# Optimization experiments

Hardware: AMD Instinct MI355X
Metric: run time of the kernel (lower is better)

## Reference

```python
import jax, jax.numpy as jnp
import numpy as np

INPUT_DIM = 512
HIDDEN_DIM = 1024
OUTPUT_DIM = 128
BATCH = 128
SEQ_LEN = 512


def setup_inputs() -> dict:
    key = jax.random.key(0)
    ks = jax.random.split(key, 8)
    s_ih = 1.0 / np.sqrt(HIDDEN_DIM)
    x = jax.random.normal(ks[0], (BATCH, SEQ_LEN, INPUT_DIM), dtype=jnp.float32)
    # LSTMCell params (PyTorch layout: [4*H, in], gate order i,f,g,o)
    W_ih = jax.random.uniform(ks[1], (4 * HIDDEN_DIM, INPUT_DIM), jnp.float32, -s_ih, s_ih)
    W_hh = jax.random.uniform(ks[2], (4 * HIDDEN_DIM, HIDDEN_DIM), jnp.float32, -s_ih, s_ih)
    b_ih = jax.random.uniform(ks[3], (4 * HIDDEN_DIM,), jnp.float32, -s_ih, s_ih)
    b_hh = jax.random.uniform(ks[4], (4 * HIDDEN_DIM,), jnp.float32, -s_ih, s_ih)
    # fc: Linear(hidden_dim, output_dim)
    s_fc = 1.0 / np.sqrt(HIDDEN_DIM)
    W_fc = jax.random.uniform(ks[5], (OUTPUT_DIM, HIDDEN_DIM), jnp.float32, -s_fc, s_fc)
    b_fc = jax.random.uniform(ks[6], (OUTPUT_DIM,), jnp.float32, -s_fc, s_fc)
    return {"x": x, "W_ih": W_ih, "W_hh": W_hh, "b_ih": b_ih, "b_hh": b_hh,
            "W_fc": W_fc, "b_fc": b_fc}


def _lstm_forward(x, W_ih, W_hh, b_ih, b_hh):
    B = x.shape[0]
    H = W_hh.shape[1]
    # Precompute input projections for all timesteps: [S, B, 4H]
    x_proj = jnp.einsum('bsi,gi->sbg', x, W_ih) + b_ih + b_hh

    def step(carry, xp_t):
        h, c = carry
        gates = xp_t + h @ W_hh.T  # [B, 4H]
        i, f, g, o = jnp.split(gates, 4, axis=-1)
        i = jax.nn.sigmoid(i)
        f = jax.nn.sigmoid(f)
        g = jnp.tanh(g)
        o = jax.nn.sigmoid(o)
        c = f * c + i * g
        h = o * jnp.tanh(c)
        return (h, c), None

    h0 = jnp.zeros((B, H), x.dtype)
    c0 = jnp.zeros((B, H), x.dtype)
    (hn, cn), _ = jax.lax.scan(step, (h0, c0), x_proj)
    return hn


def reference(x, W_ih, W_hh, b_ih, b_hh, W_fc, b_fc):
    hn = _lstm_forward(x, W_ih, W_hh, b_ih, b_hh)
    return hn @ W_fc.T + b_fc
```

## Files before the change

### kernel.cpp

```cpp
#include <hip/hip_runtime.h>
#include <hip/hip_bf16.h>

#define B_   128
#define S_   512
#define I_   512
#define H_   1024
#define G_   4096
#define O_   128
#define NWG  256
#define HU   8

typedef short bf16x8 __attribute__((ext_vector_type(8)));
typedef float f32x4  __attribute__((ext_vector_type(4)));
typedef unsigned short u16;
typedef unsigned long long u64;

__device__ __forceinline__ u16 f2bf(float f){
  union { float f; unsigned u; } v; v.f = f;
  unsigned r = v.u + 0x7fffu + ((v.u >> 16) & 1u);
  return (u16)(r >> 16);
}
__device__ __forceinline__ float sigm(float x){ return 1.0f/(1.0f + __expf(-x)); }
__device__ __forceinline__ float tanhfast(float x){ return 1.0f - 2.0f/(1.0f + __expf(2.0f*x)); }

__device__ __forceinline__ void coh_store64(u16* p, u64 v){
  __hip_atomic_store((u64*)p, v, __ATOMIC_RELAXED, __HIP_MEMORY_SCOPE_AGENT);
}
__device__ __forceinline__ u64 coh_load64(const void* p){
  return __hip_atomic_load((const u64*)p, __ATOMIC_RELAXED, __HIP_MEMORY_SCOPE_AGENT);
}

#define HL(dst, boff) \
  asm volatile("global_load_dwordx4 %0, %1, off offset:" boff " sc0 sc1" \
               : "=v"(dst) : "v"(haddr) : "memory");

#define MF(a,b,c) __builtin_amdgcn_mfma_f32_16x16x32_bf16((a),(b),(c),0,0,0)

__global__ void cast_f32_bf16(const float* __restrict__ src, u16* __restrict__ dst, int n4){
  int i = blockIdx.x*blockDim.x + threadIdx.x;
  const int st = gridDim.x*blockDim.x;
  for (; i < n4; i += st){
    float4 v = ((const float4*)src)[i];
    ushort4 o = make_ushort4(f2bf(v.x), f2bf(v.y), f2bf(v.z), f2bf(v.w));
    ((ushort4*)dst)[i] = o;
  }
}

__global__ void prep_bias(const float* __restrict__ bih, const float* __restrict__ bhh,
                          float* __restrict__ bc){
  int i = blockIdx.x*blockDim.x + threadIdx.x;
  if (i < G_) bc[i] = bih[i] + bhh[i];
}

__shared__ u16 wih_s[32*520];
__shared__ u16 whh_s[32*1032];

__global__ __launch_bounds__(256) void lstm_persist(
    const u16*   __restrict__ xbf,
    const float* __restrict__ xf,
    const int use_xbf,
    const u16*   __restrict__ Wih,
    const u16*   __restrict__ Whh,
    const float* __restrict__ bias,
    u16*         __restrict__ hbuf,
    float*       __restrict__ hfin,
    const float* __restrict__ Wfc,
    const float* __restrict__ bfc,
    float*       __restrict__ out,
    unsigned*    __restrict__ bar)
{
  const int wg = blockIdx.x, tid = threadIdx.x;
  const int bh = wg >> 7;
  const int cg = wg & 127;
  const int wv = tid >> 6, lane = tid & 63;
  const int n = lane & 15, g4 = lane >> 4;
  const int u0 = cg * HU;
  const int rb = bh*64 + wv*16;

  auto colmap = [&](int lc){ return (((lc>>4)<<1) + ((lc&15)>>3))*H_ + u0 + (lc&7); };

  for (int idx = tid; idx < 32*64; idx += 256){
    int lc = idx >> 6, c8 = (idx & 63) * 8;
    *(bf16x8*)(&wih_s[lc*520 + c8]) = *(const bf16x8*)(Wih + (size_t)colmap(lc)*I_ + c8);
  }
  for (int idx = tid; idx < 32*128; idx += 256){
    int lc = idx >> 7, c8 = (idx & 127) * 8;
    *(bf16x8*)(&whh_s[lc*1032 + c8]) = *(const bf16x8*)(Whh + (size_t)colmap(lc)*H_ + c8);
  }
  if (tid < 64){
    u16* p = hbuf + (size_t)(bh*64 + tid)*H_ + u0;
    coh_store64(p, 0ull); coh_store64(p + 4, 0ull);
  }
  asm volatile("s_waitcnt vmcnt(0)" ::: "memory");
  __syncthreads();
  if (tid == 0) __hip_atomic_fetch_add(bar, 1u, __ATOMIC_RELAXED, __HIP_MEMORY_SCOPE_AGENT);

  const float bias0 = bias[(0*2 + (n>>3))*H_ + u0 + (n&7)];
  const float bias1 = bias[(1*2 + (n>>3))*H_ + u0 + (n&7)];
  float cst[4] = {0.f, 0.f, 0.f, 0.f};
  const int hi = (n >> 3);
  const f32x4 z = {0.f,0.f,0.f,0.f};
  f32x4 ax0, ax1;

  auto xpart = [&](int t){
    ax0 = z; ax1 = z;
    if (use_xbf){
      const u16* xr = xbf + (size_t)(rb + n)*(S_*I_) + (size_t)t*I_;
      #pragma unroll 4
      for (int ks = 0; ks < 16; ++ks){
        const int kk = ks*32 + g4*8;
        bf16x8 a  = *(const bf16x8*)(xr + kk);
        bf16x8 b0 = *(const bf16x8*)(&wih_s[n*520 + kk]);
        bf16x8 b1 = *(const bf16x8*)(&wih_s[(16+n)*520 + kk]);
        ax0 = MF(a, b0, ax0); ax1 = MF(a, b1, ax1);
      }
    } else {
      const float* xr = xf + (size_t)(rb + n)*(S_*I_) + (size_t)t*I_;
      #pragma unroll 2
      for (int ks = 0; ks < 16; ++ks){
        const int kk = ks*32 + g4*8;
        float4 va = *(const float4*)(xr + kk), vb = *(const float4*)(xr + kk + 4);
        bf16x8 a;
        a[0]=(short)f2bf(va.x); a[1]=(short)f2bf(va.y); a[2]=(short)f2bf(va.z); a[3]=(short)f2bf(va.w);
        a[4]=(short)f2bf(vb.x); a[5]=(short)f2bf(vb.y); a[6]=(short)f2bf(vb.z); a[7]=(short)f2bf(vb.w);
        bf16x8 b0 = *(const bf16x8*)(&wih_s[n*520 + kk]);
        bf16x8 b1 = *(const bf16x8*)(&wih_s[(16+n)*520 + kk]);
        ax0 = MF(a, b0, ax0); ax1 = MF(a, b1, ax1);
      }
    }
  };

  xpart(0);
  unsigned tgt = NWG;

  for (int t = 0; t < S_; ++t){
    const u16* __restrict__ hc = hbuf + (size_t)(t & 1)*(B_*H_);
    u16*       __restrict__ hn = hbuf + (size_t)((t+1) & 1)*(B_*H_);

    if (tid == 0){
      while (__hip_atomic_load(bar, __ATOMIC_RELAXED, __HIP_MEMORY_SCOPE_AGENT) < tgt)
        __builtin_amdgcn_s_sleep(1);
    }
    __syncthreads();

    const u16* haddr = hc + (size_t)(rb + n)*H_ + g4*8;
    f32x4 acc0a = ax0, acc1a = ax1, acc0b = z, acc1b = z;
    bf16x8 hA0,hA1,hA2,hA3,hA4,hA5,hA6,hA7;
    bf16x8 hB0,hB1,hB2,hB3,hB4,hB5,hB6,hB7;

    #define CONS(hreg, ks) { \
      const int kk = (ks)*32 + g4*8; \
      bf16x8 bf0 = *(const bf16x8*)(&whh_s[n*1032 + kk]); \
      bf16x8 bf1 = *(const bf16x8*)(&whh_s[(16+n)*1032 + kk]); \
      if ((ks) & 1){ acc0b = MF(hreg, bf0, acc0b); acc1b = MF(hreg, bf1, acc1b); } \
      else         { acc0a = MF(hreg, bf0, acc0a); acc1a = MF(hreg, bf1, acc1a); } }
    #define CONS8(P, base) \
      CONS(P##0, (base)+0) CONS(P##1, (base)+1) CONS(P##2, (base)+2) CONS(P##3, (base)+3) \
      CONS(P##4, (base)+4) CONS(P##5, (base)+5) CONS(P##6, (base)+6) CONS(P##7, (base)+7)

    HL(hA0,"0")    HL(hA1,"64")   HL(hA2,"128")  HL(hA3,"192")
    HL(hA4,"256")  HL(hA5,"320")  HL(hA6,"384")  HL(hA7,"448")
    HL(hB0,"512")  HL(hB1,"576")  HL(hB2,"640")  HL(hB3,"704")
    HL(hB4,"768")  HL(hB5,"832")  HL(hB6,"896")  HL(hB7,"960")

    asm volatile("s_waitcnt vmcnt(8)" ::: "memory");
    __builtin_amdgcn_sched_barrier(0);
    CONS8(hA, 0)
    HL(hA0,"1024") HL(hA1,"1088") HL(hA2,"1152") HL(hA3,"1216")
    HL(hA4,"1280") HL(hA5,"1344") HL(hA6,"1408") HL(hA7,"1472")

    asm volatile("s_waitcnt vmcnt(8)" ::: "memory");
    __builtin_amdgcn_sched_barrier(0);
    CONS8(hB, 8)
    HL(hB0,"1536") HL(hB1,"1600") HL(hB2,"1664") HL(hB3,"1728")
    HL(hB4,"1792") HL(hB5,"1856") HL(hB6,"1920") HL(hB7,"1984")

    asm volatile("s_waitcnt vmcnt(8)" ::: "memory");
    __builtin_amdgcn_sched_barrier(0);
    CONS8(hA, 16)

    asm volatile("s_waitcnt vmcnt(0)" ::: "memory");
    __builtin_amdgcn_sched_barrier(0);
    CONS8(hB, 24)

    #undef CONS8
    #undef CONS

    f32x4 acc0 = acc0a + acc0b;
    f32x4 acc1 = acc1a + acc1b;

    #pragma unroll
    for (int reg = 0; reg < 4; ++reg){
      float p0 = acc0[reg] + bias0;
      float p1 = acc1[reg] + bias1;
      float q0 = __shfl_xor(p0, 8);
      float q1 = __shfl_xor(p1, 8);
      float ip = hi ? q0 : p0;
      float fp = hi ? p0 : q0;
      float gp = hi ? q1 : p1;
      float op = hi ? p1 : q1;
      float iv = sigm(ip), fv = sigm(fp), gv = tanhfast(gp), ov = sigm(op);
      float c = fv*cst[reg] + iv*gv;
      cst[reg] = c;
      float h = ov * tanhfast(c);
      const int r = rb + g4*4 + reg;

      unsigned v16 = f2bf(h);
      unsigned pr  = v16 | (__shfl_xor(v16, 1) << 16);
      unsigned pr2 = __shfl_xor(pr, 2);
      if (hi == 0 && (n & 3) == 0){
        u64 q = (u64)pr | ((u64)pr2 << 32);
        coh_store64(hn + (size_t)r*H_ + u0 + n, q);
      }
      if (t == S_-1){
        unsigned fb = __float_as_uint(h);
        unsigned fo = __shfl_xor(fb, 1);
        if (hi == 0 && (n & 1) == 0){
          u64 q = (u64)fb | ((u64)fo << 32);
          __hip_atomic_store((u64*)(hfin + (size_t)r*H_ + u0 + n), q,
                             __ATOMIC_RELAXED, __HIP_MEMORY_SCOPE_AGENT);
        }
      }
    }

    asm volatile("s_waitcnt vmcnt(0)" ::: "memory");
    __syncthreads();
    if (tid == 0) __hip_atomic_fetch_add(bar, 1u, __ATOMIC_RELAXED, __HIP_MEMORY_SCOPE_AGENT);
    tgt += NWG;

    if (t < S_-1) xpart(t+1);
  }

  if (tid == 0){
    while (__hip_atomic_load(bar, __ATOMIC_RELAXED, __HIP_MEMORY_SCOPE_AGENT) < tgt)
      __builtin_amdgcn_s_sleep(1);
  }
  __syncthreads();

  {
    const int b = wg & 127;
    const int o = (wg >> 7)*64 + (tid >> 2);
    const int qtr = tid & 3;
    const float* hb = hfin + (size_t)b*H_ + qtr*256;
    const float* wb = Wfc + (size_t)o*H_ + qtr*256;
    float s = 0.f;
    #pragma unroll 8
    for (int j = 0; j < 128; ++j){
      u64 q = coh_load64(hb + j*2);
      float a0 = __uint_as_float((unsigned)q);
      float a1 = __uint_as_float((unsigned)(q >> 32));
      float2 w = *(const float2*)(wb + j*2);
      s += a0*w.x + a1*w.y;
    }
    s += __shfl_xor(s, 1);
    s += __shfl_xor(s, 2);
    if (qtr == 0) out[(size_t)b*O_ + o] = s + bfc[o];
  }
}

extern "C" void kernel_launch(void* const* d_in, const int* in_sizes, int n_in,
                              void* d_out, int out_size, void* d_ws, size_t ws_size,
                              hipStream_t stream) {
  const float* x   = (const float*)d_in[0];
  const float* Wih = (const float*)d_in[1];
  const float* Whh = (const float*)d_in[2];
  const float* bih = (const float*)d_in[3];
  const float* bhh = (const float*)d_in[4];
  const float* Wfc = (const float*)d_in[5];
  const float* bfc = (const float*)d_in[6];
  float* out = (float*)d_out;

  char* ws = (char*)d_ws;
  u16*      wih_bf = (u16*)     (ws + 0);
  u16*      whh_bf = (u16*)     (ws + 4194304);
  float*    biasc  = (float*)   (ws + 12582912);
  u16*      hbuf   = (u16*)     (ws + 12599296);
  float*    hfin   = (float*)   (ws + 13123584);
  unsigned* bar    = (unsigned*)(ws + 13647872);
  u16*      xbf    = (u16*)     (ws + 13648128);
  const int use_xbf = (ws_size >= (size_t)13648128 + 67108864) ? 1 : 0;

  hipMemsetAsync(bar, 0, 256, stream);
  cast_f32_bf16<<<1024, 256, 0, stream>>>(Wih, wih_bf, (G_*I_)/4);
  cast_f32_bf16<<<2048, 256, 0, stream>>>(Whh, whh_bf, (G_*H_)/4);
  prep_bias<<<16, 256, 0, stream>>>(bih, bhh, biasc);
  if (use_xbf)
    cast_f32_bf16<<<2048, 256, 0, stream>>>(x, xbf, (B_*S_*I_)/4);

  lstm_persist<<<NWG, 256, 0, stream>>>(xbf, x, use_xbf, wih_bf, whh_bf, biasc,
                                        hbuf, hfin, Wfc, bfc, out, bar);
}
```

Measured before the change: 4.748 ms.

## Replace atomic-counter grid barrier with per-workgroup flags and issue all h loads upfront

The single global counter that all 256 workgroups atomically incremented each timestep is replaced by one flag per workgroup. Each workgroup stores its step number into its own flag, and all 256 threads poll one flag each, combining the results with a wave-wide __all. This removes contention on a single atomic address in the per-step grid barrier. Separately, all 32 hidden-state loads are now issued before any MFMA, using staged vmcnt waits, which deepens memory-level parallelism at the cost of more VGPRs.

```diff
diff --git a/kernel.cpp b/kernel.cpp
--- a/kernel.cpp
+++ b/kernel.cpp
@@ -67,7 +67,7 @@
     const float* __restrict__ Wfc,
     const float* __restrict__ bfc,
     float*       __restrict__ out,
-    unsigned*    __restrict__ bar)
+    unsigned*    __restrict__ flags)
 {
   const int wg = blockIdx.x, tid = threadIdx.x;
   const int bh = wg >> 7;
@@ -79,6 +79,16 @@
 
   auto colmap = [&](int lc){ return (((lc>>4)<<1) + ((lc&15)>>3))*H_ + u0 + (lc&7); };
 
+  const unsigned* myflag = flags + (wv<<6) + lane;
+  auto waitbar = [&](unsigned tgt){
+    unsigned f = __hip_atomic_load(myflag, __ATOMIC_RELAXED, __HIP_MEMORY_SCOPE_AGENT);
+    while (!__all((int)(f >= tgt))){
+      __builtin_amdgcn_s_sleep(1);
+      f = __hip_atomic_load(myflag, __ATOMIC_RELAXED, __HIP_MEMORY_SCOPE_AGENT);
+    }
+    __syncthreads();
+  };
+
   for (int idx = tid; idx < 32*64; idx += 256){
     int lc = idx >> 6, c8 = (idx & 63) * 8;
     *(bf16x8*)(&wih_s[lc*520 + c8]) = *(const bf16x8*)(Wih + (size_t)colmap(lc)*I_ + c8);
@@ -93,7 +103,8 @@
   }
   asm volatile("s_waitcnt vmcnt(0)" ::: "memory");
   __syncthreads();
-  if (tid == 0) __hip_atomic_fetch_add(bar, 1u, __ATOMIC_RELAXED, __HIP_MEMORY_SCOPE_AGENT);
+  unsigned arr = 1;
+  if (tid == 0) __hip_atomic_store(&flags[wg], arr, __ATOMIC_RELAXED, __HIP_MEMORY_SCOPE_AGENT);
 
   const float bias0 = bias[(0*2 + (n>>3))*H_ + u0 + (n&7)];
   const float bias1 = bias[(1*2 + (n>>3))*H_ + u0 + (n&7)];
@@ -131,22 +142,19 @@
   };
 
   xpart(0);
-  unsigned tgt = NWG;
 
   for (int t = 0; t < S_; ++t){
     const u16* __restrict__ hc = hbuf + (size_t)(t & 1)*(B_*H_);
     u16*       __restrict__ hn = hbuf + (size_t)((t+1) & 1)*(B_*H_);
 
-    if (tid == 0){
-      while (__hip_atomic_load(bar, __ATOMIC_RELAXED, __HIP_MEMORY_SCOPE_AGENT) < tgt)
-        __builtin_amdgcn_s_sleep(1);
-    }
-    __syncthreads();
+    waitbar(arr);
 
     const u16* haddr = hc + (size_t)(rb + n)*H_ + g4*8;
     f32x4 acc0a = ax0, acc1a = ax1, acc0b = z, acc1b = z;
     bf16x8 hA0,hA1,hA2,hA3,hA4,hA5,hA6,hA7;
     bf16x8 hB0,hB1,hB2,hB3,hB4,hB5,hB6,hB7;
+    bf16x8 hC0,hC1,hC2,hC3,hC4,hC5,hC6,hC7;
+    bf16x8 hD0,hD1,hD2,hD3,hD4,hD5,hD6,hD7;
 
     #define CONS(hreg, ks) { \
       const int kk = (ks)*32 + g4*8; \
@@ -162,26 +170,23 @@
     HL(hA4,"256")  HL(hA5,"320")  HL(hA6,"384")  HL(hA7,"448")
     HL(hB0,"512")  HL(hB1,"576")  HL(hB2,"640")  HL(hB3,"704")
     HL(hB4,"768")  HL(hB5,"832")  HL(hB6,"896")  HL(hB7,"960")
-
+    HL(hC0,"1024") HL(hC1,"1088") HL(hC2,"1152") HL(hC3,"1216")
+    HL(hC4,"1280") HL(hC5,"1344") HL(hC6,"1408") HL(hC7,"1472")
+    HL(hD0,"1536") HL(hD1,"1600") HL(hD2,"1664") HL(hD3,"1728")
+    HL(hD4,"1792") HL(hD5,"1856") HL(hD6,"1920") HL(hD7,"1984")
+
+    asm volatile("s_waitcnt vmcnt(24)" ::: "memory");
+    __builtin_amdgcn_sched_barrier(0);
+    CONS8(hA, 0)
+    asm volatile("s_waitcnt vmcnt(16)" ::: "memory");
+    __builtin_amdgcn_sched_barrier(0);
+    CONS8(hB, 8)
     asm volatile("s_waitcnt vmcnt(8)" ::: "memory");
     __builtin_amdgcn_sched_barrier(0);
-    CONS8(hA, 0)
-    HL(hA0,"1024") HL(hA1,"1088") HL(hA2,"1152") HL(hA3,"1216")
-    HL(hA4,"1280") HL(hA5,"1344") HL(hA6,"1408") HL(hA7,"1472")
-
-    asm volatile("s_waitcnt vmcnt(8)" ::: "memory");
-    __builtin_amdgcn_sched_barrier(0);
-    CONS8(hB, 8)
-    HL(hB0,"1536") HL(hB1,"1600") HL(hB2,"1664") HL(hB3,"1728")
-    HL(hB4,"1792") HL(hB5,"1856") HL(hB6,"1920") HL(hB7,"1984")
-
-    asm volatile("s_waitcnt vmcnt(8)" ::: "memory");
-    __builtin_amdgcn_sched_barrier(0);
-    CONS8(hA, 16)
-
+    CONS8(hC, 16)
     asm volatile("s_waitcnt vmcnt(0)" ::: "memory");
     __builtin_amdgcn_sched_barrier(0);
-    CONS8(hB, 24)
+    CONS8(hD, 24)
 
     #undef CONS8
     #undef CONS
@@ -225,17 +230,13 @@
 
     asm volatile("s_waitcnt vmcnt(0)" ::: "memory");
     __syncthreads();
-    if (tid == 0) __hip_atomic_fetch_add(bar, 1u, __ATOMIC_RELAXED, __HIP_MEMORY_SCOPE_AGENT);
-    tgt += NWG;
+    ++arr;
+    if (tid == 0) __hip_atomic_store(&flags[wg], arr, __ATOMIC_RELAXED, __HIP_MEMORY_SCOPE_AGENT);
 
     if (t < S_-1) xpart(t+1);
   }
 
-  if (tid == 0){
-    while (__hip_atomic_load(bar, __ATOMIC_RELAXED, __HIP_MEMORY_SCOPE_AGENT) < tgt)
-      __builtin_amdgcn_s_sleep(1);
-  }
-  __syncthreads();
+  waitbar(arr);
 
   {
     const int b = wg & 127;
@@ -276,11 +277,11 @@
   float*    biasc  = (float*)   (ws + 12582912);
   u16*      hbuf   = (u16*)     (ws + 12599296);
   float*    hfin   = (float*)   (ws + 13123584);
-  unsigned* bar    = (unsigned*)(ws + 13647872);
-  u16*      xbf    = (u16*)     (ws + 13648128);
-  const int use_xbf = (ws_size >= (size_t)13648128 + 67108864) ? 1 : 0;
-
-  hipMemsetAsync(bar, 0, 256, stream);
+  unsigned* flags  = (unsigned*)(ws + 13647872);
+  u16*      xbf    = (u16*)     (ws + 13648896);
+  const int use_xbf = (ws_size >= (size_t)13648896 + 67108864) ? 1 : 0;
+
+  hipMemsetAsync(flags, 0, 1024, stream);
   cast_f32_bf16<<<1024, 256, 0, stream>>>(Wih, wih_bf, (G_*I_)/4);
   cast_f32_bf16<<<2048, 256, 0, stream>>>(Whh, whh_bf, (G_*H_)/4);
   prep_bias<<<16, 256, 0, stream>>>(bih, bhh, biasc);
@@ -288,5 +289,5 @@
     cast_f32_bf16<<<2048, 256, 0, stream>>>(x, xbf, (B_*S_*I_)/4);
 
   lstm_persist<<<NWG, 256, 0, stream>>>(xbf, x, use_xbf, wih_bf, whh_bf, biasc,
-                                        hbuf, hfin, Wfc, bfc, out, bar);
-}
+                                        hbuf, hfin, Wfc, bfc, out, flags);
+}
```

New measurement: 4.699 ms. Within noise of the previous version (-1.0%).
